# Performance work log

Measured on AMD Instinct MI355X. Metric: run time of the kernel, lower is better.

Reference implementation:

```python
import jax, jax.numpy as jnp
import numpy as np

DN = ('NCHW', 'OIHW', 'NCHW')
TEMP = 3.0
EPS = 1e-5


def conv2d(x, w, b):
    y = jax.lax.conv_general_dilated(x, w, (1, 1), 'SAME', dimension_numbers=DN)
    return y + b[None, :, None, None]


def cp_conv4d(x, wq, bq, wsp, bsp):
    # CenterPivotConv4d: 2D conv over query dims (h,w) batched over support dims,
    # plus 2D conv over support dims (hs,ws) batched over query dims.
    B, C, h, w, hs, ws = x.shape
    x1 = x.transpose(0, 4, 5, 1, 2, 3).reshape(B * hs * ws, C, h, w)
    o1 = conv2d(x1, wq, bq)
    Co = o1.shape[1]
    o1 = o1.reshape(B, hs, ws, Co, h, w).transpose(0, 3, 4, 5, 1, 2)
    x2 = x.transpose(0, 2, 3, 1, 4, 5).reshape(B * h * w, C, hs, ws)
    o2 = conv2d(x2, wsp, bsp)
    o2 = o2.reshape(B, h, w, Co, hs, ws).transpose(0, 3, 1, 2, 4, 5)
    return o1 + o2


def conv_stack(x, params):
    for wq, bq, wsp, bsp in params:  # fixed 3 layers, structurally distinct channels
        x = jax.nn.relu(cp_conv4d(x, wq, bq, wsp, bsp))
    return x


def neigh_consensus(x, params):
    # symmetric_mode: conv(x) + conv(x with (h,w)<->(hs,ws) swapped), swapped back
    y1 = conv_stack(x, params)
    y2 = conv_stack(x.transpose(0, 1, 4, 5, 2, 3), params).transpose(0, 1, 4, 5, 2, 3)
    return y1 + y2


def mutual_matching(c):
    # c: [B, 1, f1, f2, f3, f4]; ch==1 so the torch views reduce to axis maxes
    b_max = jnp.max(c, axis=(1, 2, 3), keepdims=True)  # max over (ch,f1,f2) per (f3,f4)
    a_max = jnp.max(c, axis=(4, 5), keepdims=True)     # max over (f3,f4) per (f1,f2)
    return c * (c / (a_max + EPS)) * (c / (b_max + EPS))


def matchnet_fwd(corr, v, ig_mask, params):
    B, _, h, w, hs, ws = corr.shape
    c = mutual_matching(corr)
    c = neigh_consensus(c, params)
    c = mutual_matching(c)
    corr2d = c.reshape(B, h * w, hs * ws)
    mask = jnp.broadcast_to(ig_mask.reshape(B, -1, hs * ws), corr2d.shape)
    corr2d = jnp.where(mask, jnp.float32(1e-4), corr2d)
    attn = jax.nn.softmax(corr2d * TEMP, axis=-1)
    # bmm(v, attn^T): v [B,Cv,K], attn [B,Q,K] -> [B,Cv,Q]
    wv = jnp.einsum('bck,bqk->bcq', v, attn)
    return wv.reshape(B, -1, h, w)


def setup_inputs():
    key = jax.random.key(0)
    ks = jax.random.split(key, 16)
    B, h, w, hs, ws, Cv = 4, 32, 32, 32, 32, 256
    chans = [(1, 10), (10, 10), (10, 1)]
    inp = {
        'corr': jax.random.normal(ks[0], (B, 1, h, w, hs, ws), jnp.float32),
        'v': jax.random.normal(ks[1], (B, Cv, hs * ws), jnp.float32),
        'ig_mask': jax.random.bernoulli(ks[2], 0.1, (B, 1, hs * ws)),
    }
    i = 3
    for li, (ci, co) in enumerate(chans):
        inp[f'wq{li}'] = jax.random.normal(ks[i], (co, ci, 3, 3), jnp.float32) * 0.1; i += 1
        inp[f'bq{li}'] = jax.random.normal(ks[i], (co,), jnp.float32) * 0.01; i += 1
        inp[f'ws{li}'] = jax.random.normal(ks[i], (co, ci, 3, 3), jnp.float32) * 0.1; i += 1
        inp[f'bs{li}'] = jax.random.normal(ks[i], (co,), jnp.float32) * 0.01; i += 1
    return inp


def reference(corr, v, ig_mask, wq0, bq0, ws0, bs0, wq1, bq1, ws1, bs1, wq2, bq2, ws2, bs2):
    params = [(wq0, bq0, ws0, bs0), (wq1, bq1, ws1, bs1), (wq2, bq2, ws2, bs2)]
    return matchnet_fwd(corr, v, ig_mask, params)
```

## Files before the change

### kernel.cpp

```cpp
#include <hip/hip_runtime.h>
#include <hip/hip_bf16.h>
#include <cstdint>

#define TEMPF 3.0f
#define EPSF 1e-5f

typedef __attribute__((ext_vector_type(8))) short bf16x8;
typedef __attribute__((ext_vector_type(4))) float f32x4;

static __device__ __forceinline__ float bf2f(unsigned short u){
  union { unsigned u32; float f; } x; x.u32 = ((unsigned)u) << 16; return x.f;
}
static __device__ __forceinline__ unsigned short f2bf(float f){
  unsigned u = __float_as_uint(f);
  unsigned r = (u + 0x7fffu + ((u >> 16) & 1u)) >> 16;
  return (unsigned short)r;
}
static __device__ __forceinline__ float4 ld4(const float* p){ return *(const float4*)p; }
static __device__ __forceinline__ float4 ld4(const __hip_bfloat16* p){
  ushort4 u = *(const ushort4*)p;
  return make_float4(bf2f(u.x), bf2f(u.y), bf2f(u.z), bf2f(u.w));
}
static __device__ __forceinline__ void st4(float* p, float4 v){ *(float4*)p = v; }
static __device__ __forceinline__ void st4(__hip_bfloat16* p, float4 v){
  *(ushort4*)p = make_ushort4(f2bf(v.x), f2bf(v.y), f2bf(v.z), f2bf(v.w));
}

static __device__ __forceinline__ unsigned fkey(float f){
  unsigned u = __float_as_uint(f);
  return (u & 0x80000000u) ? ~u : (u | 0x80000000u);
}
static __device__ __forceinline__ float fdec(unsigned k){
  return (k & 0x80000000u) ? __uint_as_float(k ^ 0x80000000u) : __uint_as_float(~k);
}

__device__ __forceinline__ float blockMax256(float v){
  __shared__ float red[4];
  #pragma unroll
  for(int off = 32; off; off >>= 1) v = fmaxf(v, __shfl_down(v, off));
  __syncthreads();
  if((threadIdx.x & 63) == 0) red[threadIdx.x >> 6] = v;
  __syncthreads();
  return fmaxf(fmaxf(red[0], red[1]), fmaxf(red[2], red[3]));
}
__device__ __forceinline__ float blockSum256(float v){
  __shared__ float red2[4];
  #pragma unroll
  for(int off = 32; off; off >>= 1) v += __shfl_down(v, off);
  __syncthreads();
  if((threadIdx.x & 63) == 0) red2[threadIdx.x >> 6] = v;
  __syncthreads();
  return red2[0] + red2[1] + red2[2] + red2[3];
}

__global__ __launch_bounds__(256) void setup_k(
    const unsigned* __restrict__ mask, int* __restrict__ flag,
    unsigned* __restrict__ cb1, unsigned* __restrict__ cb2, unsigned* __restrict__ zeros,
    const float* __restrict__ wq1, const float* __restrict__ wsp1,
    const float* __restrict__ bq1, const float* __restrict__ bsp1,
    unsigned short* __restrict__ wp, float* __restrict__ bs){
  const int b = blockIdx.x, tid = threadIdx.x;
  if(b == 0){
    __shared__ int sa, sb;
    if(tid == 0){ sa = 0; sb = 0; }
    __syncthreads();
    int a = 0, b2 = 0;
    for(int i = tid; i < 1024; i += 256){
      unsigned w = mask[i];
      if(w != 0u && w != 1u) a = 1;
      if(w != 0u && w != 0x3f800000u) b2 = 1;
    }
    if(a)  atomicOr(&sa, 1);
    if(b2) atomicOr(&sb, 1);
    __syncthreads();
    if(tid == 0) *flag = (sa == 0) ? 0 : ((sb == 0) ? 1 : 2);
  } else if(b < 25){
    int i = (b - 1) * 256 + tid;
    if(i < 6144){
      int path = i / 3072, rem = i % 3072, co = rem / 192, k = rem % 192;
      float v = 0.f;
      if(co < 10 && k < 180){
        const float* WA = path ? wsp1 : wq1;
        const float* WB = path ? wq1 : wsp1;
        int kk = k < 90 ? k : k - 90;
        int ci = kk / 9, t = kk % 9;
        v = (k < 90 ? WA : WB)[(co * 10 + ci) * 9 + t];
      }
      wp[i] = f2bf(v);
    }
    if(i < 32){
      int co = i & 15;
      bs[i] = co < 10 ? bq1[co] + bsp1[co] : 0.f;
    }
  } else {
    int i = (b - 25) * 256 + tid;
    if(i < 4096){ cb1[i] = 0u; cb2[i] = 0u; }
    if(i < 1024) zeros[i] = 0u;
  }
}

__global__ __launch_bounds__(256) void rcmax_k(const float* __restrict__ x,
    float* __restrict__ rmax, unsigned* __restrict__ cbits){
  const int b = blockIdx.x, tid = threadIdx.x;
  if(b < 4096){
    float4 v = *(const float4*)(x + (size_t)b * 1024 + tid * 4);
    float m = fmaxf(fmaxf(v.x, v.y), fmaxf(v.z, v.w));
    m = blockMax256(m);
    if(tid == 0) rmax[b] = m;
  } else {
    int blk = b - 4096;
    int bb = blk >> 5, rg = blk & 31;
    const float* base = x + (size_t)bb * 1048576 + (size_t)rg * 32 * 1024;
    int col = tid * 4;
    float4 m = make_float4(-1e30f, -1e30f, -1e30f, -1e30f);
    for(int r = 0; r < 32; ++r){
      float4 v = *(const float4*)(base + r * 1024 + col);
      m.x = fmaxf(m.x, v.x); m.y = fmaxf(m.y, v.y);
      m.z = fmaxf(m.z, v.z); m.w = fmaxf(m.w, v.w);
    }
    unsigned* cb = cbits + (bb << 10) + col;
    atomicMax(cb + 0, fkey(m.x)); atomicMax(cb + 1, fkey(m.y));
    atomicMax(cb + 2, fkey(m.z)); atomicMax(cb + 3, fkey(m.w));
  }
}

__global__ __launch_bounds__(256) void rcsum_k(const float* __restrict__ ya,
    const float* __restrict__ yb2, float* __restrict__ rmax, unsigned* __restrict__ cbits){
  const int b = blockIdx.x, tid = threadIdx.x;
  if(b < 4096){
    float4 v = *(const float4*)(ya + (size_t)b * 1024 + tid * 4);
    float4 u = *(const float4*)(yb2 + (size_t)b * 1024 + tid * 4);
    v.x += u.x; v.y += u.y; v.z += u.z; v.w += u.w;
    float m = fmaxf(fmaxf(v.x, v.y), fmaxf(v.z, v.w));
    m = blockMax256(m);
    if(tid == 0) rmax[b] = m;
  } else {
    int blk = b - 4096;
    int bb = blk >> 5, rg = blk & 31;
    const float* basea = ya  + (size_t)bb * 1048576 + (size_t)rg * 32 * 1024;
    const float* baseb = yb2 + (size_t)bb * 1048576 + (size_t)rg * 32 * 1024;
    int col = tid * 4;
    float4 m = make_float4(-1e30f, -1e30f, -1e30f, -1e30f);
    for(int r = 0; r < 32; ++r){
      float4 v = *(const float4*)(basea + r * 1024 + col);
      float4 u = *(const float4*)(baseb + r * 1024 + col);
      v.x += u.x; v.y += u.y; v.z += u.z; v.w += u.w;
      m.x = fmaxf(m.x, v.x); m.y = fmaxf(m.y, v.y);
      m.z = fmaxf(m.z, v.z); m.w = fmaxf(m.w, v.w);
    }
    unsigned* cb = cbits + (bb << 10) + col;
    atomicMax(cb + 0, fkey(m.x)); atomicMax(cb + 1, fkey(m.y));
    atomicMax(cb + 2, fkey(m.z)); atomicMax(cb + 3, fkey(m.w));
  }
}

__global__ __launch_bounds__(256) void mmapply_k(const float* __restrict__ x,
    const float* __restrict__ rmax, const unsigned* __restrict__ cbits,
    float* __restrict__ out){
  int idx4 = blockIdx.x * 256 + threadIdx.x;
  int b = idx4 >> 18;
  int rem = idx4 & 262143;
  int q = rem >> 8;
  int k = (rem & 255) * 4;
  float4 v = ((const float4*)x)[idx4];
  float ra = rmax[(b << 10) + q] + EPSF;
  const unsigned* cb = cbits + (b << 10) + k;
  float4 o;
  o.x = v.x * v.x * v.x / (ra * (fdec(cb[0]) + EPSF));
  o.y = v.y * v.y * v.y / (ra * (fdec(cb[1]) + EPSF));
  o.z = v.z * v.z * v.z / (ra * (fdec(cb[2]) + EPSF));
  o.w = v.w * v.w * v.w / (ra * (fdec(cb[3]) + EPSF));
  ((float4*)out)[idx4] = o;
}

__global__ __launch_bounds__(256)
void convmm_k(const unsigned short* __restrict__ gin, unsigned short* __restrict__ gout,
              const unsigned short* __restrict__ wpack, const float* __restrict__ bias,
              unsigned inElem, unsigned outElem, unsigned zeroElem){
  __shared__ unsigned short sh[13600];
  const int tid = threadIdx.x;
  const int blk = ((blockIdx.x & 7) << 8) | (blockIdx.x >> 3);
  const int path = blk >> 10;
  const int hw = blk & 1023;
  const int h = hw >> 5, w = hw & 31;
  const unsigned inB = inElem + (unsigned)path * 10485760u;
  const unsigned outB = outElem + (unsigned)path * 10485760u;

  for(int i = tid; i < 6800; i += 256) ((unsigned*)sh)[i] = 0u;
  __syncthreads();
  for(int idx = tid; idx < 2560; idx += 256){
    int ci = idx >> 8, s = (idx & 255) * 4;
    ushort4 v = *(const ushort4*)(gin + inB + ci * 1048576 + hw * 1024 + s);
    *(ushort4*)(sh + ci * 1360 + (1 + (s >> 5)) * 40 + 4 + (s & 31)) = v;
  }
  __syncthreads();

  const int l = tid & 63, wv = tid >> 6;
  const int g = l >> 4, n = l & 15;

  bf16x8 af[6];
  #pragma unroll
  for(int sl = 0; sl < 6; ++sl)
    af[sl] = *(const bf16x8*)(wpack + ((size_t)path * 16 + n) * 192 + sl * 32 + g * 8);
  f32x4 cb = *(const f32x4*)(bias + path * 16 + g * 4);

  unsigned b1i[24]; unsigned b2b[32]; unsigned msk2[4], msk5[4];
  const unsigned s0 = (unsigned)wv * 256u;
  #pragma unroll
  for(int gg = 0; gg < 4; ++gg){
    if(g == gg){
      #pragma unroll
      for(int sl = 0; sl < 3; ++sl){
        #pragma unroll
        for(int j = 0; j < 8; ++j){
          const int k = sl * 32 + gg * 8 + j;
          unsigned v = zeroElem;
          if(k < 90){
            const int ci = k / 9, t = k % 9;
            const int hh = h + t / 3 - 1, ww = w + t % 3 - 1;
            if((unsigned)hh < 32u && (unsigned)ww < 32u)
              v = inB + (unsigned)ci * 1048576u + (unsigned)((hh * 32 + ww) * 1024) + (unsigned)n;
          }
          b1i[sl * 8 + j] = (v + s0) * 2u;
        }
      }
      #pragma unroll
      for(int sl = 2; sl < 6; ++sl){
        #pragma unroll
        for(int j = 0; j < 8; ++j){
          const int k = sl * 32 + gg * 8 + j;
          const int kp = (k >= 90 && k < 180) ? (k - 90) : 0;
          const int ci = kp / 9, t = kp % 9;
          b2b[(sl - 2) * 8 + j] = (unsigned)(ci * 1360 + (t / 3) * 40 + 3 + (t % 3) + n);
        }
      }
      #pragma unroll
      for(int p = 0; p < 4; ++p){
        const int ka = 64 + gg * 8 + 2 * p, kb = ka + 1;
        msk2[p] = ((ka >= 90) ? 0xFFFFu : 0u) | ((kb >= 90) ? 0xFFFF0000u : 0u);
        const int kc = 160 + gg * 8 + 2 * p, kd = kc + 1;
        msk5[p] = ((kc < 180) ? 0xFFFFu : 0u) | ((kd < 180) ? 0xFFFF0000u : 0u);
      }
    }
  }

  unsigned sb[4]; bool sv[4];
  #pragma unroll
  for(int r = 0; r < 4; ++r){
    const int co = g * 4 + r;
    sv[r] = (co < 10);
    sb[r] = (outB + (unsigned)co * 1048576u + (unsigned)(hw * 1024) + s0 + (unsigned)n) * 2u;
  }
  unsigned rowcs = (s0 >> 5) * 40u;

  const char* ginc = (const char*)gin;
  char* goutc = (char*)gout;

  unsigned short ga[24], gb[24];
  #pragma unroll
  for(int m = 0; m < 24; ++m) ga[m] = *(const unsigned short*)(ginc + b1i[m]);
  #pragma unroll
  for(int m = 0; m < 24; ++m) b1i[m] += 32u;

#define CMM_STEP(CUR, NXT, RDELTA)                                                \
  {                                                                               \
    _Pragma("unroll")                                                             \
    for(int m = 0; m < 24; ++m) NXT[m] = *(const unsigned short*)(ginc + b1i[m]); \
    _Pragma("unroll")                                                             \
    for(int m = 0; m < 24; ++m) b1i[m] += 32u;                                    \
    union { unsigned u[4]; bf16x8 v; } B0, B1, B2, B3, B4, B5;                    \
    _Pragma("unroll")                                                             \
    for(int p = 0; p < 4; ++p){                                                   \
      B0.u[p] = (unsigned)CUR[2*p]    | ((unsigned)CUR[2*p+1] << 16);             \
      B1.u[p] = (unsigned)CUR[8+2*p]  | ((unsigned)CUR[8+2*p+1] << 16);           \
      unsigned glo = (unsigned)CUR[16+2*p] | ((unsigned)CUR[16+2*p+1] << 16);     \
      unsigned llo = (unsigned)sh[b2b[2*p] + rowcs] |                             \
                     ((unsigned)sh[b2b[2*p+1] + rowcs] << 16);                    \
      B2.u[p] = glo | (llo & msk2[p]);                                            \
      B3.u[p] = (unsigned)sh[b2b[8+2*p]  + rowcs] |                               \
                ((unsigned)sh[b2b[8+2*p+1]  + rowcs] << 16);                      \
      B4.u[p] = (unsigned)sh[b2b[16+2*p] + rowcs] |                               \
                ((unsigned)sh[b2b[16+2*p+1] + rowcs] << 16);                      \
      B5.u[p] = ((unsigned)sh[b2b[24+2*p] + rowcs] |                              \
                 ((unsigned)sh[b2b[24+2*p+1] + rowcs] << 16)) & msk5[p];          \
    }                                                                             \
    rowcs += (RDELTA);                                                            \
    __builtin_amdgcn_s_setprio(1);                                                \
    f32x4 acc = __builtin_amdgcn_mfma_f32_16x16x32_bf16(af[0], B0.v, cb, 0, 0, 0);\
    acc = __builtin_amdgcn_mfma_f32_16x16x32_bf16(af[1], B1.v, acc, 0, 0, 0);     \
    acc = __builtin_amdgcn_mfma_f32_16x16x32_bf16(af[2], B2.v, acc, 0, 0, 0);     \
    acc = __builtin_amdgcn_mfma_f32_16x16x32_bf16(af[3], B3.v, acc, 0, 0, 0);     \
    acc = __builtin_amdgcn_mfma_f32_16x16x32_bf16(af[4], B4.v, acc, 0, 0, 0);     \
    acc = __builtin_amdgcn_mfma_f32_16x16x32_bf16(af[5], B5.v, acc, 0, 0, 0);     \
    __builtin_amdgcn_s_setprio(0);                                                \
    _Pragma("unroll")                                                             \
    for(int r = 0; r < 4; ++r){                                                   \
      if(sv[r])                                                                   \
        *(unsigned short*)(goutc + sb[r]) = f2bf(fmaxf(acc[r], 0.f));             \
    }                                                                             \
    _Pragma("unroll")                                                             \
    for(int r = 0; r < 4; ++r) sb[r] += 32u;                                      \
  }

  for(int itp = 0; itp < 8; ++itp){
    CMM_STEP(ga, gb, 16u)
    CMM_STEP(gb, ga, 24u)
  }
#undef CMM_STEP
}

template<int CI, typename TI, typename TO>
__global__ __launch_bounds__(128, 4) void conv12_k(
    const TI* __restrict__ in, TO* __restrict__ out,
    const float* __restrict__ wq, const float* __restrict__ wsp,
    const float* __restrict__ bq, const float* __restrict__ bsp,
    size_t in_pstride){
  __shared__ float P[18][36];
  const int tid = threadIdx.x;
  const int blk = ((blockIdx.x & 7) << 9) | (blockIdx.x >> 3);
  const int path = blk >> 11;
  const int r0 = blk & 2047;
  const int strip = r0 & 1;
  const int hw = r0 >> 1;
  const int w = hw & 31, h = hw >> 5;
  const int lr = tid >> 3;
  const int c  = (tid & 7) * 4;
  const int own = hw * 1024 + strip * 512 + tid * 4;
  const int halo_src = hw * 1024 + (strip ? 15 * 32 : 16 * 32) + (tid & 7) * 4;
  const int hrow = strip ? 0 : 17;
  const float* wA = path ? wsp : wq;
  const float* wB = path ? wq : wsp;
  const TI* inp = in + (size_t)path * in_pstride;
  TO* outp = out + (size_t)path * 10485760;

  bool valid[9];
  #pragma unroll
  for(int dh = 0; dh < 3; ++dh)
    #pragma unroll
    for(int dw = 0; dw < 3; ++dw)
      valid[dh * 3 + dw] = ((unsigned)(h + dh - 1) < 32u) && ((unsigned)(w + dw - 1) < 32u);

  for(int i = tid; i < 18 * 36; i += 128) ((float*)P)[i] = 0.f;

  float acc[10][4];
  #pragma unroll
  for(int co = 0; co < 10; ++co){
    float bv = bq[co] + bsp[co];
    acc[co][0] = bv; acc[co][1] = bv; acc[co][2] = bv; acc[co][3] = bv;
  }

  for(int ci = 0; ci < CI; ++ci){
    const TI* base = inp + (size_t)ci * 1048576;
    float4 qv[9];
    #pragma unroll
    for(int dh = 0; dh < 3; ++dh){
      #pragma unroll
      for(int dw = 0; dw < 3; ++dw){
        const int t = dh * 3 + dw;
        float4 vv = make_float4(0.f, 0.f, 0.f, 0.f);
        if(valid[t]) vv = ld4(base + own + ((dh - 1) * 32 + (dw - 1)) * 1024);
        qv[t] = vv;
      }
    }
    float4 hv = make_float4(0.f, 0.f, 0.f, 0.f);
    if(tid < 8) hv = ld4(base + halo_src);

    __syncthreads();
    *(float4*)&P[1 + lr][c] = qv[4];
    if(tid < 8) *(float4*)&P[hrow][tid * 4] = hv;
    __syncthreads();

    float pr[3][6];
    #pragma unroll
    for(int k1 = 0; k1 < 3; ++k1){
      const float* row = &P[lr + k1][0];
      float4 mid = *(const float4*)(row + c);
      pr[k1][0] = row[c == 0 ? 32 : c - 1];
      pr[k1][1] = mid.x; pr[k1][2] = mid.y; pr[k1][3] = mid.z; pr[k1][4] = mid.w;
      pr[k1][5] = row[c + 4];
    }

    #pragma unroll
    for(int co = 0; co < 10; ++co){
      const float* wa = wA + (co * CI + ci) * 9;
      const float* wb = wB + (co * CI + ci) * 9;
      #pragma unroll
      for(int t = 0; t < 9; ++t){
        float wv = wa[t];
        acc[co][0] += wv * qv[t].x; acc[co][1] += wv * qv[t].y;
        acc[co][2] += wv * qv[t].z; acc[co][3] += wv * qv[t].w;
      }
      #pragma unroll
      for(int k1 = 0; k1 < 3; ++k1){
        #pragma unroll
        for(int k2 = 0; k2 < 3; ++k2){
          float wv = wb[k1 * 3 + k2];
          #pragma unroll
          for(int j = 0; j < 4; ++j) acc[co][j] += wv * pr[k1][k2 + j];
        }
      }
    }
  }

  #pragma unroll
  for(int co = 0; co < 10; ++co){
    float4 r;
    r.x = fmaxf(acc[co][0], 0.f); r.y = fmaxf(acc[co][1], 0.f);
    r.z = fmaxf(acc[co][2], 0.f); r.w = fmaxf(acc[co][3], 0.f);
    st4(outp + (size_t)co * 1048576 + own, r);
  }
}

__global__ __launch_bounds__(128, 4) void conv3_k(
    const __hip_bfloat16* __restrict__ in,
    const float* __restrict__ wq, const float* __restrict__ wsp,
    const float* __restrict__ bq, const float* __restrict__ bsp,
    float* __restrict__ y0b, float* __restrict__ y1b){
  __shared__ float P[18][36];
  const int tid = threadIdx.x;
  const int blk = ((blockIdx.x & 7) << 9) | (blockIdx.x >> 3);
  const int path = blk >> 11;
  const int r0 = blk & 2047;
  const int strip = r0 & 1;
  const int hw = r0 >> 1;
  const int w = hw & 31, h = hw >> 5;
  const int lr = tid >> 3;
  const int c  = (tid & 7) * 4;
  const int own = hw * 1024 + strip * 512 + tid * 4;
  const int halo_src = hw * 1024 + (strip ? 15 * 32 : 16 * 32) + (tid & 7) * 4;
  const int hrow = strip ? 0 : 17;
  const float* wA = path ? wsp : wq;
  const float* wB = path ? wq : wsp;
  const __hip_bfloat16* inp = in + (size_t)path * 10485760;
  float* yout = path ? y1b : y0b;

  bool valid[9];
  #pragma unroll
  for(int dh = 0; dh < 3; ++dh)
    #pragma unroll
    for(int dw = 0; dw < 3; ++dw)
      valid[dh * 3 + dw] = ((unsigned)(h + dh - 1) < 32u) && ((unsigned)(w + dw - 1) < 32u);

  for(int i = tid; i < 18 * 36; i += 128) ((float*)P)[i] = 0.f;

  float bv = bq[0] + bsp[0];
  float a0 = bv, a1 = bv, a2 = bv, a3 = bv;

  for(int ci = 0; ci < 10; ++ci){
    const __hip_bfloat16* base = inp + (size_t)ci * 1048576;
    float4 qv[9];
    #pragma unroll
    for(int dh = 0; dh < 3; ++dh){
      #pragma unroll
      for(int dw = 0; dw < 3; ++dw){
        const int t = dh * 3 + dw;
        float4 vv = make_float4(0.f, 0.f, 0.f, 0.f);
        if(valid[t]) vv = ld4(base + own + ((dh - 1) * 32 + (dw - 1)) * 1024);
        qv[t] = vv;
      }
    }
    float4 hv = make_float4(0.f, 0.f, 0.f, 0.f);
    if(tid < 8) hv = ld4(base + halo_src);

    __syncthreads();
    *(float4*)&P[1 + lr][c] = qv[4];
    if(tid < 8) *(float4*)&P[hrow][tid * 4] = hv;
    __syncthreads();

    float pr[3][6];
    #pragma unroll
    for(int k1 = 0; k1 < 3; ++k1){
      const float* row = &P[lr + k1][0];
      float4 mid = *(const float4*)(row + c);
      pr[k1][0] = row[c == 0 ? 32 : c - 1];
      pr[k1][1] = mid.x; pr[k1][2] = mid.y; pr[k1][3] = mid.z; pr[k1][4] = mid.w;
      pr[k1][5] = row[c + 4];
    }

    const float* wa = wA + ci * 9;
    const float* wb = wB + ci * 9;
    #pragma unroll
    for(int t = 0; t < 9; ++t){
      float wv = wa[t];
      a0 += wv * qv[t].x; a1 += wv * qv[t].y;
      a2 += wv * qv[t].z; a3 += wv * qv[t].w;
    }
    #pragma unroll
    for(int k1 = 0; k1 < 3; ++k1){
      #pragma unroll
      for(int k2 = 0; k2 < 3; ++k2){
        float wv = wb[k1 * 3 + k2];
        a0 += wv * pr[k1][k2 + 0];
        a1 += wv * pr[k1][k2 + 1];
        a2 += wv * pr[k1][k2 + 2];
        a3 += wv * pr[k1][k2 + 3];
      }
    }
  }

  float4 r;
  r.x = fmaxf(a0, 0.f); r.y = fmaxf(a1, 0.f);
  r.z = fmaxf(a2, 0.f); r.w = fmaxf(a3, 0.f);
  *(float4*)(yout + own) = r;
}

__global__ __launch_bounds__(256) void softmax_k(
    const float* __restrict__ y, const float* __restrict__ y2,
    const float* __restrict__ rmax,
    const unsigned* __restrict__ cbits, const void* __restrict__ mask,
    const int* __restrict__ mode, float* __restrict__ attn){
  int row = blockIdx.x;
  int b = row >> 10;
  int tid = threadIdx.x;
  int kc = tid * 4;
  float ra = rmax[row] + EPSF;
  float4 v = *(const float4*)(y  + (size_t)row * 1024 + kc);
  float4 u = *(const float4*)(y2 + (size_t)row * 1024 + kc);
  v.x += u.x; v.y += u.y; v.z += u.z; v.w += u.w;
  int md = *mode;
  float vv[4] = {v.x, v.y, v.z, v.w};
  float s[4];
  #pragma unroll
  for(int j = 0; j < 4; ++j){
    int k = kc + j;
    float cb = fdec(cbits[(b << 10) + k]) + EPSF;
    float m = vv[j] * vv[j] * vv[j] / (ra * cb);
    bool msk;
    if(md == 0)      msk = ((const int*)mask)[(b << 10) + k] != 0;
    else if(md == 1) msk = ((const float*)mask)[(b << 10) + k] != 0.f;
    else             msk = ((const unsigned char*)mask)[(b << 10) + k] != 0;
    if(msk) m = 1e-4f;
    s[j] = m * TEMPF;
  }
  float mx = fmaxf(fmaxf(s[0], s[1]), fmaxf(s[2], s[3]));
  mx = blockMax256(mx);
  float e[4]; float sum = 0.f;
  #pragma unroll
  for(int j = 0; j < 4; ++j){ e[j] = expf(s[j] - mx); sum += e[j]; }
  sum = blockSum256(sum);
  float inv = 1.0f / sum;
  float4 o; o.x = e[0] * inv; o.y = e[1] * inv; o.z = e[2] * inv; o.w = e[3] * inv;
  *(float4*)(attn + (size_t)row * 1024 + kc) = o;
}

__global__ __launch_bounds__(256) void bmm_k(const float* __restrict__ v,
    const float* __restrict__ attn, float* __restrict__ part){
  __shared__ float At[64][68];
  __shared__ float Bt[64][68];
  int b  = blockIdx.y >> 2;
  int ks = blockIdx.y & 3;
  int ct = blockIdx.x >> 4, qt = blockIdx.x & 15;
  int tid = threadIdx.x;
  int c0 = ct * 64, q0 = qt * 64;
  int tx = tid & 15, ty = tid >> 4;
  float acc[4][4] = {};
  for(int k0 = ks * 256; k0 < ks * 256 + 256; k0 += 64){
    #pragma unroll
    for(int l = 0; l < 4; ++l){
      int r = (tid >> 4) + l * 16;
      int cc = (tid & 15) * 4;
      *(float4*)&At[r][cc] = *(const float4*)(v    + ((size_t)b * 256  + c0 + r) * 1024 + k0 + cc);
      *(float4*)&Bt[r][cc] = *(const float4*)(attn + ((size_t)b * 1024 + q0 + r) * 1024 + k0 + cc);
    }
    __syncthreads();
    #pragma unroll 4
    for(int kk = 0; kk < 64; ++kk){
      float a_[4], b_[4];
      #pragma unroll
      for(int i = 0; i < 4; ++i){ a_[i] = At[ty * 4 + i][kk]; b_[i] = Bt[tx * 4 + i][kk]; }
      #pragma unroll
      for(int i = 0; i < 4; ++i)
        #pragma unroll
        for(int j = 0; j < 4; ++j) acc[i][j] += a_[i] * b_[j];
    }
    __syncthreads();
  }
  float* pb = part + (size_t)ks * 1048576;
  #pragma unroll
  for(int i = 0; i < 4; ++i){
    float4 r; r.x = acc[i][0]; r.y = acc[i][1]; r.z = acc[i][2]; r.w = acc[i][3];
    *(float4*)(pb + ((size_t)b * 256 + c0 + ty * 4 + i) * 1024 + q0 + tx * 4) = r;
  }
}

__global__ __launch_bounds__(256) void bmmred_k(const float* __restrict__ part,
                                                float* __restrict__ out){
  int i = blockIdx.x * 256 + threadIdx.x;
  const float4* p = (const float4*)part;
  float4 a = p[i], b = p[i + 262144], cc = p[i + 524288], d = p[i + 786432];
  float4 o;
  o.x = a.x + b.x + cc.x + d.x;
  o.y = a.y + b.y + cc.y + d.y;
  o.z = a.z + b.z + cc.z + d.z;
  o.w = a.w + b.w + cc.w + d.w;
  ((float4*)out)[i] = o;
}

extern "C" void kernel_launch(void* const* d_in, const int* in_sizes, int n_in,
                              void* d_out, int out_size, void* d_ws, size_t ws_size,
                              hipStream_t stream){
  (void)in_sizes; (void)n_in; (void)out_size; (void)ws_size;
  const float* corr = (const float*)d_in[0];
  const float* v    = (const float*)d_in[1];
  const void*  mask = d_in[2];
  const float* wq[3]  = {(const float*)d_in[3],  (const float*)d_in[7],  (const float*)d_in[11]};
  const float* bq[3]  = {(const float*)d_in[4],  (const float*)d_in[8],  (const float*)d_in[12]};
  const float* wsp[3] = {(const float*)d_in[5],  (const float*)d_in[9],  (const float*)d_in[13]};
  const float* bsp[3] = {(const float*)d_in[6],  (const float*)d_in[10], (const float*)d_in[14]};
  float* out = (float*)d_out;

  char* ws = (char*)d_ws;
  float* x0 = (float*)(ws);
  float* y  = (float*)(ws + 16777216);
  char* aux = ws + 33554432;
  float*    rmax1 = (float*)(aux);
  unsigned* cb1   = (unsigned*)(aux + 16384);
  float*    rmax2 = (float*)(aux + 32768);
  unsigned* cb2   = (unsigned*)(aux + 49152);
  int*      flag  = (int*)(aux + 65536);
  unsigned short* wp = (unsigned short*)(aux + 69632);
  float*          bs = (float*)(aux + 81920);
  unsigned* zeros = (unsigned*)(aux + 98304);
  char* treg = ws + 33685504;
  __hip_bfloat16* t1 = (__hip_bfloat16*)(treg);
  __hip_bfloat16* t2 = (__hip_bfloat16*)(treg + 41943040);
  float* attn = x0;
  float* part = (float*)treg;

  const unsigned t1Elem   = 33685504u / 2u;
  const unsigned t2Elem   = 75628544u / 2u;
  const unsigned zeroElem = 33652736u / 2u;

  setup_k<<<41, 256, 0, stream>>>((const unsigned*)mask, flag, cb1, cb2, zeros,
                                  wq[1], wsp[1], bq[1], bsp[1], wp, bs);
  rcmax_k<<<4224, 256, 0, stream>>>(corr, rmax1, cb1);
  mmapply_k<<<4096, 256, 0, stream>>>(corr, rmax1, cb1, x0);

  for(int bb = 0; bb < 4; ++bb){
    const float* xb = x0 + (size_t)bb * 1048576;
    float*       yb  = y  + (size_t)bb * 1048576;
    float*       y2b = x0 + (size_t)bb * 1048576;
    conv12_k<1, float, __hip_bfloat16><<<4096, 128, 0, stream>>>(
        xb, t1, wq[0], wsp[0], bq[0], bsp[0], 0);
    convmm_k<<<2048, 256, 0, stream>>>(
        (const unsigned short*)ws, (unsigned short*)ws, wp, bs, t1Elem, t2Elem, zeroElem);
    conv3_k<<<4096, 128, 0, stream>>>(
        t2, wq[2], wsp[2], bq[2], bsp[2], yb, y2b);
  }

  rcsum_k<<<4224, 256, 0, stream>>>(y, x0, rmax2, cb2);
  softmax_k<<<4096, 256, 0, stream>>>(y, x0, rmax2, cb2, mask, flag, attn);
  bmm_k<<<dim3(64, 16), 256, 0, stream>>>(v, attn, part);
  bmmred_k<<<1024, 256, 0, stream>>>(part, out);
}
```

Measured before the change: 619.6 us.

## Fuse layer-2 conv of one batch with layer-0 conv of the next

Adds a combined kernel whose even blocks run the final 4D conv layer for batch bb and whose odd blocks run the first conv layer for batch bb+1. The first layer's conv moves out of the per-batch loop: it is launched once before the loop, then folded into the next batch's final-layer launch. The layer-0 body is specialised for a single input channel. This removes three kernel launches and overlaps the cheap layer-0 work with the layer-2 work. The cost is more blocks per launch and a reliance on the t1/t2 and x0 slices not overlapping.

Result: slower. 807.9 us (+30.4%).

```diff
diff --git a/kernel.cpp b/kernel.cpp
--- a/kernel.cpp
+++ b/kernel.cpp
@@ -309,15 +309,10 @@
 #undef CMM_STEP
 }
 
-template<int CI, typename TI, typename TO>
-__global__ __launch_bounds__(128, 4) void conv12_k(
-    const TI* __restrict__ in, TO* __restrict__ out,
-    const float* __restrict__ wq, const float* __restrict__ wsp,
-    const float* __restrict__ bq, const float* __restrict__ bsp,
-    size_t in_pstride){
-  __shared__ float P[18][36];
-  const int tid = threadIdx.x;
-  const int blk = ((blockIdx.x & 7) << 9) | (blockIdx.x >> 3);
+static __device__ __forceinline__ void l0_body(float (*P)[36], int blk, int tid,
+    const float* __restrict__ xb, __hip_bfloat16* __restrict__ t1,
+    const float* __restrict__ wq0, const float* __restrict__ wsp0,
+    const float* __restrict__ bq0, const float* __restrict__ bsp0){
   const int path = blk >> 11;
   const int r0 = blk & 2047;
   const int strip = r0 & 1;
@@ -328,10 +323,9 @@
   const int own = hw * 1024 + strip * 512 + tid * 4;
   const int halo_src = hw * 1024 + (strip ? 15 * 32 : 16 * 32) + (tid & 7) * 4;
   const int hrow = strip ? 0 : 17;
-  const float* wA = path ? wsp : wq;
-  const float* wB = path ? wq : wsp;
-  const TI* inp = in + (size_t)path * in_pstride;
-  TO* outp = out + (size_t)path * 10485760;
+  const float* wA = path ? wsp0 : wq0;
+  const float* wB = path ? wq0 : wsp0;
+  __hip_bfloat16* outp = t1 + (size_t)path * 10485760;
 
   bool valid[9];
   #pragma unroll
@@ -345,59 +339,56 @@
   float acc[10][4];
   #pragma unroll
   for(int co = 0; co < 10; ++co){
-    float bv = bq[co] + bsp[co];
+    float bv = bq0[co] + bsp0[co];
     acc[co][0] = bv; acc[co][1] = bv; acc[co][2] = bv; acc[co][3] = bv;
   }
 
-  for(int ci = 0; ci < CI; ++ci){
-    const TI* base = inp + (size_t)ci * 1048576;
-    float4 qv[9];
-    #pragma unroll
-    for(int dh = 0; dh < 3; ++dh){
-      #pragma unroll
-      for(int dw = 0; dw < 3; ++dw){
-        const int t = dh * 3 + dw;
-        float4 vv = make_float4(0.f, 0.f, 0.f, 0.f);
-        if(valid[t]) vv = ld4(base + own + ((dh - 1) * 32 + (dw - 1)) * 1024);
-        qv[t] = vv;
-      }
-    }
-    float4 hv = make_float4(0.f, 0.f, 0.f, 0.f);
-    if(tid < 8) hv = ld4(base + halo_src);
-
-    __syncthreads();
-    *(float4*)&P[1 + lr][c] = qv[4];
-    if(tid < 8) *(float4*)&P[hrow][tid * 4] = hv;
-    __syncthreads();
-
-    float pr[3][6];
+  float4 qv[9];
+  #pragma unroll
+  for(int dh = 0; dh < 3; ++dh){
+    #pragma unroll
+    for(int dw = 0; dw < 3; ++dw){
+      const int t = dh * 3 + dw;
+      float4 vv = make_float4(0.f, 0.f, 0.f, 0.f);
+      if(valid[t]) vv = ld4(xb + own + ((dh - 1) * 32 + (dw - 1)) * 1024);
+      qv[t] = vv;
+    }
+  }
+  float4 hv = make_float4(0.f, 0.f, 0.f, 0.f);
+  if(tid < 8) hv = ld4(xb + halo_src);
+
+  __syncthreads();
+  *(float4*)&P[1 + lr][c] = qv[4];
+  if(tid < 8) *(float4*)&P[hrow][tid * 4] = hv;
+  __syncthreads();
+
+  float pr[3][6];
+  #pragma unroll
+  for(int k1 = 0; k1 < 3; ++k1){
+    const float* row = &P[lr + k1][0];
+    float4 mid = *(const float4*)(row + c);
+    pr[k1][0] = row[c == 0 ? 32 : c - 1];
+    pr[k1][1] = mid.x; pr[k1][2] = mid.y; pr[k1][3] = mid.z; pr[k1][4] = mid.w;
+    pr[k1][5] = row[c + 4];
+  }
+
+  #pragma unroll
+  for(int co = 0; co < 10; ++co){
+    const float* wa = wA + co * 9;
+    const float* wb = wB + co * 9;
+    #pragma unroll
+    for(int t = 0; t < 9; ++t){
+      float wv = wa[t];
+      acc[co][0] += wv * qv[t].x; acc[co][1] += wv * qv[t].y;
+      acc[co][2] += wv * qv[t].z; acc[co][3] += wv * qv[t].w;
+    }
     #pragma unroll
     for(int k1 = 0; k1 < 3; ++k1){
-      const float* row = &P[lr + k1][0];
-      float4 mid = *(const float4*)(row + c);
-      pr[k1][0] = row[c == 0 ? 32 : c - 1];
-      pr[k1][1] = mid.x; pr[k1][2] = mid.y; pr[k1][3] = mid.z; pr[k1][4] = mid.w;
-      pr[k1][5] = row[c + 4];
-    }
-
-    #pragma unroll
-    for(int co = 0; co < 10; ++co){
-      const float* wa = wA + (co * CI + ci) * 9;
-      const float* wb = wB + (co * CI + ci) * 9;
-      #pragma unroll
-      for(int t = 0; t < 9; ++t){
-        float wv = wa[t];
-        acc[co][0] += wv * qv[t].x; acc[co][1] += wv * qv[t].y;
-        acc[co][2] += wv * qv[t].z; acc[co][3] += wv * qv[t].w;
-      }
-      #pragma unroll
-      for(int k1 = 0; k1 < 3; ++k1){
+      #pragma unroll
+      for(int k2 = 0; k2 < 3; ++k2){
+        float wv = wb[k1 * 3 + k2];
         #pragma unroll
-        for(int k2 = 0; k2 < 3; ++k2){
-          float wv = wb[k1 * 3 + k2];
-          #pragma unroll
-          for(int j = 0; j < 4; ++j) acc[co][j] += wv * pr[k1][k2 + j];
-        }
+        for(int j = 0; j < 4; ++j) acc[co][j] += wv * pr[k1][k2 + j];
       }
     }
   }
@@ -411,14 +402,11 @@
   }
 }
 
-__global__ __launch_bounds__(128, 4) void conv3_k(
+static __device__ __forceinline__ void conv3_body(float (*P)[36], int blk, int tid,
     const __hip_bfloat16* __restrict__ in,
-    const float* __restrict__ wq, const float* __restrict__ wsp,
-    const float* __restrict__ bq, const float* __restrict__ bsp,
+    const float* __restrict__ wq2, const float* __restrict__ wsp2,
+    const float* __restrict__ bq2, const float* __restrict__ bsp2,
     float* __restrict__ y0b, float* __restrict__ y1b){
-  __shared__ float P[18][36];
-  const int tid = threadIdx.x;
-  const int blk = ((blockIdx.x & 7) << 9) | (blockIdx.x >> 3);
   const int path = blk >> 11;
   const int r0 = blk & 2047;
   const int strip = r0 & 1;
@@ -429,8 +417,8 @@
   const int own = hw * 1024 + strip * 512 + tid * 4;
   const int halo_src = hw * 1024 + (strip ? 15 * 32 : 16 * 32) + (tid & 7) * 4;
   const int hrow = strip ? 0 : 17;
-  const float* wA = path ? wsp : wq;
-  const float* wB = path ? wq : wsp;
+  const float* wA = path ? wsp2 : wq2;
+  const float* wB = path ? wq2 : wsp2;
   const __hip_bfloat16* inp = in + (size_t)path * 10485760;
   float* yout = path ? y1b : y0b;
 
@@ -443,7 +431,7 @@
 
   for(int i = tid; i < 18 * 36; i += 128) ((float*)P)[i] = 0.f;
 
-  float bv = bq[0] + bsp[0];
+  float bv = bq2[0] + bsp2[0];
   float a0 = bv, a1 = bv, a2 = bv, a3 = bv;
 
   for(int ci = 0; ci < 10; ++ci){
@@ -502,6 +490,43 @@
   r.x = fmaxf(a0, 0.f); r.y = fmaxf(a1, 0.f);
   r.z = fmaxf(a2, 0.f); r.w = fmaxf(a3, 0.f);
   *(float4*)(yout + own) = r;
+}
+
+__global__ __launch_bounds__(128, 4) void conv12_k(
+    const float* __restrict__ xb, __hip_bfloat16* __restrict__ t1,
+    const float* __restrict__ wq0, const float* __restrict__ wsp0,
+    const float* __restrict__ bq0, const float* __restrict__ bsp0){
+  __shared__ float P[18][36];
+  const int blk = ((blockIdx.x & 7) << 9) | (blockIdx.x >> 3);
+  l0_body(P, blk, threadIdx.x, xb, t1, wq0, wsp0, bq0, bsp0);
+}
+
+__global__ __launch_bounds__(128, 4) void conv3_k(
+    const __hip_bfloat16* __restrict__ in,
+    const float* __restrict__ wq2, const float* __restrict__ wsp2,
+    const float* __restrict__ bq2, const float* __restrict__ bsp2,
+    float* __restrict__ y0b, float* __restrict__ y1b){
+  __shared__ float P[18][36];
+  const int blk = ((blockIdx.x & 7) << 9) | (blockIdx.x >> 3);
+  conv3_body(P, blk, threadIdx.x, in, wq2, wsp2, bq2, bsp2, y0b, y1b);
+}
+
+__global__ __launch_bounds__(128, 4) void c3l0_k(
+    const __hip_bfloat16* __restrict__ t2,
+    const float* __restrict__ wq2, const float* __restrict__ wsp2,
+    const float* __restrict__ bq2, const float* __restrict__ bsp2,
+    float* __restrict__ y0b, float* __restrict__ y1b,
+    const float* __restrict__ xbn, __hip_bfloat16* __restrict__ t1,
+    const float* __restrict__ wq0, const float* __restrict__ wsp0,
+    const float* __restrict__ bq0, const float* __restrict__ bsp0){
+  __shared__ float P[18][36];
+  const int role = blockIdx.x & 1;
+  const int rb = blockIdx.x >> 1;
+  const int blk = ((rb & 7) << 9) | (rb >> 3);
+  if(role == 0)
+    conv3_body(P, blk, threadIdx.x, t2, wq2, wsp2, bq2, bsp2, y0b, y1b);
+  else
+    l0_body(P, blk, threadIdx.x, xbn, t1, wq0, wsp0, bq0, bsp0);
 }
 
 __global__ __launch_bounds__(256) void softmax_k(
@@ -636,16 +661,19 @@
   rcmax_k<<<4224, 256, 0, stream>>>(corr, rmax1, cb1);
   mmapply_k<<<4096, 256, 0, stream>>>(corr, rmax1, cb1, x0);
 
+  conv12_k<<<4096, 128, 0, stream>>>(x0, t1, wq[0], wsp[0], bq[0], bsp[0]);
   for(int bb = 0; bb < 4; ++bb){
-    const float* xb = x0 + (size_t)bb * 1048576;
-    float*       yb  = y  + (size_t)bb * 1048576;
-    float*       y2b = x0 + (size_t)bb * 1048576;
-    conv12_k<1, float, __hip_bfloat16><<<4096, 128, 0, stream>>>(
-        xb, t1, wq[0], wsp[0], bq[0], bsp[0], 0);
+    float* yb  = y  + (size_t)bb * 1048576;
+    float* y2b = x0 + (size_t)bb * 1048576;
     convmm_k<<<2048, 256, 0, stream>>>(
         (const unsigned short*)ws, (unsigned short*)ws, wp, bs, t1Elem, t2Elem, zeroElem);
-    conv3_k<<<4096, 128, 0, stream>>>(
-        t2, wq[2], wsp[2], bq[2], bsp[2], yb, y2b);
+    if(bb < 3){
+      const float* xbn = x0 + (size_t)(bb + 1) * 1048576;
+      c3l0_k<<<8192, 128, 0, stream>>>(t2, wq[2], wsp[2], bq[2], bsp[2], yb, y2b,
+                                       xbn, t1, wq[0], wsp[0], bq[0], bsp[0]);
+    } else {
+      conv3_k<<<4096, 128, 0, stream>>>(t2, wq[2], wsp[2], bq[2], bsp[2], yb, y2b);
+    }
   }
 
   rcsum_k<<<4224, 256, 0, stream>>>(y, x0, rmax2, cb2);
```
